# Kernel tuning notes

Measured on AMD Instinct MI355X. Metric: run time of the kernel, lower is better.

Reference implementation:

```python
import jax, jax.numpy as jnp
import numpy as np
import math

INPUT_SIZE = 512
HIDDEN_SIZE = 1024
B, T = 64, 512


def setup_inputs() -> dict:
    key = jax.random.key(0)
    ks = jax.random.split(key, 8)
    stdv = 1.0 / math.sqrt(HIDDEN_SIZE)
    def U(k, shape):
        return jax.random.uniform(k, shape, jnp.float32, -stdv, stdv)
    x = jax.random.normal(ks[0], (B, T, INPUT_SIZE), jnp.float32)
    W_i_r = U(ks[1], (HIDDEN_SIZE, INPUT_SIZE))
    W_h_r = U(ks[2], (HIDDEN_SIZE, HIDDEN_SIZE))
    W_i_z = U(ks[3], (HIDDEN_SIZE, INPUT_SIZE))
    W_h_z = U(ks[4], (HIDDEN_SIZE, HIDDEN_SIZE))
    W_i_n = U(ks[5], (HIDDEN_SIZE, INPUT_SIZE))
    W_h_n = U(ks[6], (HIDDEN_SIZE, HIDDEN_SIZE))
    zeros = jnp.zeros((HIDDEN_SIZE,), jnp.float32)
    return {
        "x": x,
        "W_i_r": W_i_r, "b_i_r": zeros, "W_h_r": W_h_r, "b_h_r": zeros,
        "W_i_z": W_i_z, "b_i_z": zeros, "W_h_z": W_h_z, "b_h_z": zeros,
        "W_i_n": W_i_n, "b_i_n": zeros, "W_h_n": W_h_n, "b_h_n": zeros,
    }


def reference(x, W_i_r, b_i_r, W_h_r, b_h_r, W_i_z, b_i_z, W_h_z, b_h_z,
              W_i_n, b_i_n, W_h_n, b_h_n):
    Bn, Tn, _ = x.shape
    # Precompute all input projections in one batched matmul each: [B,T,H]
    xr = jnp.einsum('bti,hi->bth', x, W_i_r) + b_i_r
    xz = jnp.einsum('bti,hi->bth', x, W_i_z) + b_i_z
    xn = jnp.einsum('bti,hi->bth', x, W_i_n) + b_i_n

    h0 = jnp.zeros((Bn, W_h_r.shape[0]), x.dtype)

    def step(h, inp):
        xr_t, xz_t, xn_t = inp  # each [B,H]
        r = jax.nn.sigmoid(xr_t + h @ W_h_r.T + b_h_r)
        z = jax.nn.sigmoid(xz_t + h @ W_h_z.T + b_h_z)
        n = jnp.tanh(xn_t + r * (h @ W_h_n.T + b_h_n))
        h_new = (1.0 - z) * n + z * h
        return h_new, h_new

    # scan over time: inputs transposed to [T,B,H]
    xs = (xr.transpose(1, 0, 2), xz.transpose(1, 0, 2), xn.transpose(1, 0, 2))
    _, h_seq = jax.lax.scan(step, h0, xs)
    return h_seq.transpose(1, 0, 2)  # [B,T,H]
```

## Files before the change

### kernel.cpp

```cpp
#include <hip/hip_runtime.h>
#include <math.h>


#define BB 64
#define TT 512
#define II 512
#define HH 1024
#define JB 4
#define CK 128
#define PAD 132

__device__ __forceinline__ void fma4(float4& a, const float4 xv, const float4 w) {
    a.x += xv.x * w.x;
    a.y += xv.y * w.y;
    a.z += xv.z * w.z;
    a.w += xv.w * w.w;
}

__device__ __forceinline__ void accum_chunk(
    const float* __restrict__ xsrow,
    const float* __restrict__ wr, const float* __restrict__ wz,
    const float* __restrict__ wn,
    float4& aR, float4& aZ, float4& aN)
{
#pragma unroll
    for (int k4 = 0; k4 < CK / 4; ++k4) {
        float4 xv = *(const float4*)(xsrow + k4 * 4);
        fma4(aR, xv, *(const float4*)(wr + k4 * 4));
        fma4(aZ, xv, *(const float4*)(wz + k4 * 4));
        fma4(aN, xv, *(const float4*)(wn + k4 * 4));
    }
}

__global__ __launch_bounds__(256) void gru_step(
    const float* __restrict__ x,
    const float* __restrict__ Wir, const float* __restrict__ Whr,
    const float* __restrict__ Wiz, const float* __restrict__ Whz,
    const float* __restrict__ Win, const float* __restrict__ Whn,
    const float* __restrict__ bir, const float* __restrict__ bhr,
    const float* __restrict__ biz, const float* __restrict__ bhz,
    const float* __restrict__ bin_, const float* __restrict__ bhn,
    float* __restrict__ out, int t)
{
    __shared__ float xs[BB][PAD];
    const int tid = threadIdx.x;
    const int b   = tid & 63;
    const int jg  = tid >> 6;
    const int j   = __builtin_amdgcn_readfirstlane((int)blockIdx.x * JB + jg);

    float4 aR  = {0.f, 0.f, 0.f, 0.f};
    float4 aZ  = {0.f, 0.f, 0.f, 0.f};
    float4 aXN = {0.f, 0.f, 0.f, 0.f};
    float4 aHN = {0.f, 0.f, 0.f, 0.f};

    const float* xbase = x + (size_t)t * II;
    for (int kc = 0; kc < II / CK; ++kc) {
#pragma unroll
        for (int i = 0; i < 8; ++i) {
            int f   = tid + 256 * i;
            int row = f >> 5;
            int c4  = f & 31;
            *(float4*)&xs[row][c4 * 4] =
                *(const float4*)(xbase + (size_t)row * (TT * II) + kc * CK + c4 * 4);
        }
        __syncthreads();
        accum_chunk(&xs[b][0],
                    Wir + (size_t)j * II + kc * CK,
                    Wiz + (size_t)j * II + kc * CK,
                    Win + (size_t)j * II + kc * CK,
                    aR, aZ, aXN);
        __syncthreads();
    }

    if (t > 0) {
        const float* hbase = out + (size_t)(t - 1) * HH;
        for (int kc = 0; kc < HH / CK; ++kc) {
#pragma unroll
            for (int i = 0; i < 8; ++i) {
                int f   = tid + 256 * i;
                int row = f >> 5;
                int c4  = f & 31;
                *(float4*)&xs[row][c4 * 4] =
                    *(const float4*)(hbase + (size_t)row * (TT * HH) + kc * CK + c4 * 4);
            }
            __syncthreads();
            accum_chunk(&xs[b][0],
                        Whr + (size_t)j * HH + kc * CK,
                        Whz + (size_t)j * HH + kc * CK,
                        Whn + (size_t)j * HH + kc * CK,
                        aR, aZ, aHN);
            __syncthreads();
        }
    }

    float rpre = (aR.x + aR.y + aR.z + aR.w) + bir[j] + bhr[j];
    float zpre = (aZ.x + aZ.y + aZ.z + aZ.w) + biz[j] + bhz[j];
    float hn   = (aHN.x + aHN.y + aHN.z + aHN.w) + bhn[j];
    float xn   = (aXN.x + aXN.y + aXN.z + aXN.w) + bin_[j];

    float r = 1.f / (1.f + __expf(-rpre));
    float z = 1.f / (1.f + __expf(-zpre));
    float n = tanhf(xn + r * hn);

    float hprev = (t > 0) ? out[(size_t)b * (TT * HH) + (size_t)(t - 1) * HH + j] : 0.f;
    float hnew  = (1.f - z) * n + z * hprev;
    out[(size_t)b * (TT * HH) + (size_t)t * HH + j] = hnew;
}

extern "C" void kernel_launch(void* const* d_in, const int* in_sizes, int n_in,
                              void* d_out, int out_size, void* d_ws, size_t ws_size,
                              hipStream_t stream) {
    (void)in_sizes; (void)n_in; (void)d_ws; (void)ws_size; (void)out_size;

    const float* x    = (const float*)d_in[0];
    const float* Wir  = (const float*)d_in[1];
    const float* bir  = (const float*)d_in[2];
    const float* Whr  = (const float*)d_in[3];
    const float* bhr  = (const float*)d_in[4];
    const float* Wiz  = (const float*)d_in[5];
    const float* biz  = (const float*)d_in[6];
    const float* Whz  = (const float*)d_in[7];
    const float* bhz  = (const float*)d_in[8];
    const float* Win  = (const float*)d_in[9];
    const float* bin_ = (const float*)d_in[10];
    const float* Whn  = (const float*)d_in[11];
    const float* bhn  = (const float*)d_in[12];
    float* out = (float*)d_out;

    for (int t = 0; t < TT; ++t) {
        gru_step<<<dim3(HH / JB), dim3(256), 0, stream>>>(
            x, Wir, Whr, Wiz, Whz, Win, Whn,
            bir, bhr, biz, bhz, bin_, bhn, out, t);
    }
}
```

Measured before the change: 14.14 ms.

## Use split-bf16 MFMA for GRU step with prepacked weights and inputs

Adds prep kernels that split fp32 weights and inputs into hi/lo bf16 pairs in an MFMA-friendly tiled layout. Each per-timestep step then runs 16x16x32 bf16 MFMAs, three products per pair (hi*hi, hi*lo, lo*hi), to approximate fp32 accuracy. The hidden state is double-buffered as bf16 hi/lo in workspace. This replaces scalar FMA with matrix cores and drops the LDS staging, at the cost of slightly lower precision and fewer blocks (64) per step. If the workspace is too small, it falls back to the old fp32 kernel.

Result: slower. 17.60 ms (+24.4%).

```diff
diff --git a/kernel.cpp b/kernel.cpp
--- a/kernel.cpp
+++ b/kernel.cpp
@@ -2,26 +2,200 @@
 #include <math.h>
 
 
+typedef __attribute__((ext_vector_type(8))) short short8;
+typedef __attribute__((ext_vector_type(4))) float f32x4;
+typedef unsigned short u16;
+typedef unsigned int u32;
+
+#define TT 512
 #define BB 64
-#define TT 512
 #define II 512
 #define HH 1024
-#define JB 4
+#define JT 16
+#define NBLK 64
+#define NKS 48
+#define NKS_X 16
+
+#define SZ_WPL (3ULL*64*48*512*2)
+#define OFF_WHI 0ULL
+#define OFF_WLO (OFF_WHI + SZ_WPL)
+#define SZ_XPL (512ULL*64*512*2)
+#define OFF_XHI (OFF_WLO + SZ_WPL)
+#define OFF_XLO (OFF_XHI + SZ_XPL)
+#define SZ_HPL (2ULL*64*1024*2)
+#define OFF_HHI (OFF_XLO + SZ_XPL)
+#define OFF_HLO (OFF_HHI + SZ_HPL)
+#define WS_NEEDED (OFF_HLO + SZ_HPL)
+
+__device__ __forceinline__ u16 f2bf(float f) {
+    u32 u = __float_as_uint(f);
+    u32 r = (u + 0x7FFFu + ((u >> 16) & 1u)) >> 16;
+    return (u16)r;
+}
+__device__ __forceinline__ float bf2f(u16 h) {
+    return __uint_as_float(((u32)h) << 16);
+}
+
+
+__global__ __launch_bounds__(256) void prep_w(
+    const float* __restrict__ Wir, const float* __restrict__ Whr,
+    const float* __restrict__ Wiz, const float* __restrict__ Whz,
+    const float* __restrict__ Win, const float* __restrict__ Whn,
+    u16* __restrict__ whi, u16* __restrict__ wlo)
+{
+    int id = blockIdx.x * 256 + threadIdx.x;
+    int lane = id & 63;
+    int qq = id >> 6;
+    int ks = qq % 48;
+    int rr = qq / 48;
+    int g = rr >> 6;
+    int jt = rr & 63;
+    int j = jt * 16 + (lane & 15);
+    int k = ks * 32 + (lane >> 4) * 8;
+    const float* Wi = (g == 0) ? Wir : (g == 1) ? Wiz : Win;
+    const float* Wh = (g == 0) ? Whr : (g == 1) ? Whz : Whn;
+    const float* src = (k < II) ? (Wi + (size_t)j * II + k)
+                                : (Wh + (size_t)j * HH + (k - II));
+    short8 H, L;
+#pragma unroll
+    for (int e = 0; e < 8; ++e) {
+        float f = src[e];
+        u16 hi = f2bf(f);
+        u16 lo = f2bf(f - bf2f(hi));
+        H[e] = (short)hi;
+        L[e] = (short)lo;
+    }
+    size_t dst = (size_t)qq * 512 + (size_t)lane * 8;
+    *(short8*)(whi + dst) = H;
+    *(short8*)(wlo + dst) = L;
+}
+
+__global__ __launch_bounds__(256) void prep_x(
+    const float* __restrict__ x, u16* __restrict__ xhi, u16* __restrict__ xlo)
+{
+    int id = blockIdx.x * 256 + threadIdx.x;
+    int t = id >> 12;
+    int b = (id >> 6) & 63;
+    int i8 = id & 63;
+    const float* src = x + ((size_t)b * TT + t) * II + i8 * 8;
+    short8 H, L;
+#pragma unroll
+    for (int e = 0; e < 8; ++e) {
+        float f = src[e];
+        u16 hi = f2bf(f);
+        u16 lo = f2bf(f - bf2f(hi));
+        H[e] = (short)hi;
+        L[e] = (short)lo;
+    }
+    size_t dst = ((size_t)t * 64 + b) * II + (size_t)i8 * 8;
+    *(short8*)(xhi + dst) = H;
+    *(short8*)(xlo + dst) = L;
+}
+
+
+#define LD8(p) (*(const short8*)(p))
+#define MFMA16(a, b, c) __builtin_amdgcn_mfma_f32_16x16x32_bf16((a), (b), (c), 0, 0, 0)
+
+__global__ __launch_bounds__(256) void gru_step_mfma(
+    const u16* __restrict__ xhi, const u16* __restrict__ xlo,
+    const u16* __restrict__ whi, const u16* __restrict__ wlo,
+    const u16* __restrict__ hhi_r, const u16* __restrict__ hlo_r,
+    u16* __restrict__ hhi_w, u16* __restrict__ hlo_w,
+    const float* __restrict__ bir, const float* __restrict__ bhr,
+    const float* __restrict__ biz, const float* __restrict__ bhz,
+    const float* __restrict__ bin_, const float* __restrict__ bhn,
+    float* __restrict__ out, int t)
+{
+    const int tid = threadIdx.x;
+    const int w = tid >> 6;
+    const int lane = tid & 63;
+    const int q = lane >> 4;
+    const int nn = lane & 15;
+    const int jt = blockIdx.x;
+    const int j = jt * JT + nn;
+
+    f32x4 accR = {0.f, 0.f, 0.f, 0.f};
+    f32x4 accZ = {0.f, 0.f, 0.f, 0.f};
+    f32x4 accNx = {0.f, 0.f, 0.f, 0.f};
+    f32x4 accNh = {0.f, 0.f, 0.f, 0.f};
+
+    const int rowA = w * 16 + nn;
+    const size_t GS = (size_t)64 * 48 * 512;
+    const u16* axh = xhi + ((size_t)t * 64 + rowA) * II + q * 8;
+    const u16* axl = xlo + ((size_t)t * 64 + rowA) * II + q * 8;
+    const size_t wb = (size_t)jt * 48 * 512 + (size_t)lane * 8;
+    const u16* bwh = whi + wb;
+    const u16* bwl = wlo + wb;
+
+#pragma unroll 4
+    for (int Ks = 0; Ks < NKS_X; ++Ks) {
+        short8 ah = LD8(axh + Ks * 32);
+        short8 al = LD8(axl + Ks * 32);
+        const u16* b0 = bwh + (size_t)Ks * 512;
+        const u16* l0 = bwl + (size_t)Ks * 512;
+        short8 bh, bl;
+        bh = LD8(b0);            bl = LD8(l0);
+        accR = MFMA16(ah, bh, accR); accR = MFMA16(ah, bl, accR); accR = MFMA16(al, bh, accR);
+        bh = LD8(b0 + GS);       bl = LD8(l0 + GS);
+        accZ = MFMA16(ah, bh, accZ); accZ = MFMA16(ah, bl, accZ); accZ = MFMA16(al, bh, accZ);
+        bh = LD8(b0 + 2 * GS);   bl = LD8(l0 + 2 * GS);
+        accNx = MFMA16(ah, bh, accNx); accNx = MFMA16(ah, bl, accNx); accNx = MFMA16(al, bh, accNx);
+    }
+
+    if (t > 0) {
+        const u16* ahh = hhi_r + (size_t)rowA * HH + q * 8;
+        const u16* ahl = hlo_r + (size_t)rowA * HH + q * 8;
+#pragma unroll 4
+        for (int K2 = 0; K2 < 32; ++K2) {
+            short8 ah = LD8(ahh + K2 * 32);
+            short8 al = LD8(ahl + K2 * 32);
+            const u16* b0 = bwh + (size_t)(NKS_X + K2) * 512;
+            const u16* l0 = bwl + (size_t)(NKS_X + K2) * 512;
+            short8 bh, bl;
+            bh = LD8(b0);            bl = LD8(l0);
+            accR = MFMA16(ah, bh, accR); accR = MFMA16(ah, bl, accR); accR = MFMA16(al, bh, accR);
+            bh = LD8(b0 + GS);       bl = LD8(l0 + GS);
+            accZ = MFMA16(ah, bh, accZ); accZ = MFMA16(ah, bl, accZ); accZ = MFMA16(al, bh, accZ);
+            bh = LD8(b0 + 2 * GS);   bl = LD8(l0 + 2 * GS);
+            accNh = MFMA16(ah, bh, accNh); accNh = MFMA16(ah, bl, accNh); accNh = MFMA16(al, bh, accNh);
+        }
+    }
+
+    const float vbir = bir[j], vbhr = bhr[j];
+    const float vbiz = biz[j], vbhz = bhz[j];
+    const float vbin = bin_[j], vbhn = bhn[j];
+#pragma unroll
+    for (int e = 0; e < 4; ++e) {
+        int row = w * 16 + q * 4 + e;
+        float rp = accR[e] + vbir + vbhr;
+        float zp = accZ[e] + vbiz + vbhz;
+        float hn = accNh[e] + vbhn;
+        float xn = accNx[e] + vbin;
+        float rg = 1.f / (1.f + __expf(-rp));
+        float zg = 1.f / (1.f + __expf(-zp));
+        float ng = tanhf(xn + rg * hn);
+        float hp = (t > 0) ? out[((size_t)row * TT + (t - 1)) * HH + j] : 0.f;
+        float hv = (1.f - zg) * ng + zg * hp;
+        out[((size_t)row * TT + t) * HH + j] = hv;
+        u16 hh = f2bf(hv);
+        u16 hl = f2bf(hv - bf2f(hh));
+        hhi_w[(size_t)row * HH + j] = hh;
+        hlo_w[(size_t)row * HH + j] = hl;
+    }
+}
+
+
 #define CK 128
 #define PAD 132
 
 __device__ __forceinline__ void fma4(float4& a, const float4 xv, const float4 w) {
-    a.x += xv.x * w.x;
-    a.y += xv.y * w.y;
-    a.z += xv.z * w.z;
-    a.w += xv.w * w.w;
+    a.x += xv.x * w.x; a.y += xv.y * w.y; a.z += xv.z * w.z; a.w += xv.w * w.w;
 }
 
 __device__ __forceinline__ void accum_chunk(
     const float* __restrict__ xsrow,
     const float* __restrict__ wr, const float* __restrict__ wz,
-    const float* __restrict__ wn,
-    float4& aR, float4& aZ, float4& aN)
+    const float* __restrict__ wn, float4& aR, float4& aZ, float4& aN)
 {
 #pragma unroll
     for (int k4 = 0; k4 < CK / 4; ++k4) {
@@ -32,7 +206,7 @@
     }
 }
 
-__global__ __launch_bounds__(256) void gru_step(
+__global__ __launch_bounds__(256) void gru_step_f32(
     const float* __restrict__ x,
     const float* __restrict__ Wir, const float* __restrict__ Whr,
     const float* __restrict__ Wiz, const float* __restrict__ Whz,
@@ -44,73 +218,59 @@
 {
     __shared__ float xs[BB][PAD];
     const int tid = threadIdx.x;
-    const int b   = tid & 63;
-    const int jg  = tid >> 6;
-    const int j   = __builtin_amdgcn_readfirstlane((int)blockIdx.x * JB + jg);
-
-    float4 aR  = {0.f, 0.f, 0.f, 0.f};
-    float4 aZ  = {0.f, 0.f, 0.f, 0.f};
-    float4 aXN = {0.f, 0.f, 0.f, 0.f};
-    float4 aHN = {0.f, 0.f, 0.f, 0.f};
+    const int b = tid & 63;
+    const int jg = tid >> 6;
+    const int j = __builtin_amdgcn_readfirstlane((int)blockIdx.x * 4 + jg);
+
+    float4 aR = {0,0,0,0}, aZ = {0,0,0,0}, aXN = {0,0,0,0}, aHN = {0,0,0,0};
 
     const float* xbase = x + (size_t)t * II;
     for (int kc = 0; kc < II / CK; ++kc) {
 #pragma unroll
         for (int i = 0; i < 8; ++i) {
-            int f   = tid + 256 * i;
-            int row = f >> 5;
-            int c4  = f & 31;
+            int f = tid + 256 * i; int row = f >> 5; int c4 = f & 31;
             *(float4*)&xs[row][c4 * 4] =
                 *(const float4*)(xbase + (size_t)row * (TT * II) + kc * CK + c4 * 4);
         }
         __syncthreads();
-        accum_chunk(&xs[b][0],
-                    Wir + (size_t)j * II + kc * CK,
-                    Wiz + (size_t)j * II + kc * CK,
-                    Win + (size_t)j * II + kc * CK,
+        accum_chunk(&xs[b][0], Wir + (size_t)j * II + kc * CK,
+                    Wiz + (size_t)j * II + kc * CK, Win + (size_t)j * II + kc * CK,
                     aR, aZ, aXN);
         __syncthreads();
     }
-
     if (t > 0) {
         const float* hbase = out + (size_t)(t - 1) * HH;
         for (int kc = 0; kc < HH / CK; ++kc) {
 #pragma unroll
             for (int i = 0; i < 8; ++i) {
-                int f   = tid + 256 * i;
-                int row = f >> 5;
-                int c4  = f & 31;
+                int f = tid + 256 * i; int row = f >> 5; int c4 = f & 31;
                 *(float4*)&xs[row][c4 * 4] =
                     *(const float4*)(hbase + (size_t)row * (TT * HH) + kc * CK + c4 * 4);
             }
             __syncthreads();
-            accum_chunk(&xs[b][0],
-                        Whr + (size_t)j * HH + kc * CK,
-                        Whz + (size_t)j * HH + kc * CK,
-                        Whn + (size_t)j * HH + kc * CK,
+            accum_chunk(&xs[b][0], Whr + (size_t)j * HH + kc * CK,
+                        Whz + (size_t)j * HH + kc * CK, Whn + (size_t)j * HH + kc * CK,
                         aR, aZ, aHN);
             __syncthreads();
         }
     }
-
     float rpre = (aR.x + aR.y + aR.z + aR.w) + bir[j] + bhr[j];
     float zpre = (aZ.x + aZ.y + aZ.z + aZ.w) + biz[j] + bhz[j];
-    float hn   = (aHN.x + aHN.y + aHN.z + aHN.w) + bhn[j];
-    float xn   = (aXN.x + aXN.y + aXN.z + aXN.w) + bin_[j];
-
+    float hn = (aHN.x + aHN.y + aHN.z + aHN.w) + bhn[j];
+    float xn = (aXN.x + aXN.y + aXN.z + aXN.w) + bin_[j];
     float r = 1.f / (1.f + __expf(-rpre));
     float z = 1.f / (1.f + __expf(-zpre));
     float n = tanhf(xn + r * hn);
-
     float hprev = (t > 0) ? out[(size_t)b * (TT * HH) + (size_t)(t - 1) * HH + j] : 0.f;
-    float hnew  = (1.f - z) * n + z * hprev;
+    float hnew = (1.f - z) * n + z * hprev;
     out[(size_t)b * (TT * HH) + (size_t)t * HH + j] = hnew;
 }
+
 
 extern "C" void kernel_launch(void* const* d_in, const int* in_sizes, int n_in,
                               void* d_out, int out_size, void* d_ws, size_t ws_size,
                               hipStream_t stream) {
-    (void)in_sizes; (void)n_in; (void)d_ws; (void)ws_size; (void)out_size;
+    (void)in_sizes; (void)n_in; (void)out_size;
 
     const float* x    = (const float*)d_in[0];
     const float* Wir  = (const float*)d_in[1];
@@ -127,9 +287,34 @@
     const float* bhn  = (const float*)d_in[12];
     float* out = (float*)d_out;
 
+    if (ws_size < WS_NEEDED) {
+        for (int t = 0; t < TT; ++t) {
+            gru_step_f32<<<dim3(HH / 4), dim3(256), 0, stream>>>(
+                x, Wir, Whr, Wiz, Whz, Win, Whn,
+                bir, bhr, biz, bhz, bin_, bhn, out, t);
+        }
+        return;
+    }
+
+    unsigned char* ws = (unsigned char*)d_ws;
+    u16* whi = (u16*)(ws + OFF_WHI);
+    u16* wlo = (u16*)(ws + OFF_WLO);
+    u16* xhi = (u16*)(ws + OFF_XHI);
+    u16* xlo = (u16*)(ws + OFF_XLO);
+    u16* hhi = (u16*)(ws + OFF_HHI);
+    u16* hlo = (u16*)(ws + OFF_HLO);
+
+    prep_w<<<dim3(589824 / 256), dim3(256), 0, stream>>>(
+        Wir, Whr, Wiz, Whz, Win, Whn, whi, wlo);
+    prep_x<<<dim3(2097152 / 256), dim3(256), 0, stream>>>(x, xhi, xlo);
+
     for (int t = 0; t < TT; ++t) {
-        gru_step<<<dim3(HH / JB), dim3(256), 0, stream>>>(
-            x, Wir, Whr, Wiz, Whz, Win, Whn,
+        int wp = t & 1;
+        int rp = wp ^ 1;
+        gru_step_mfma<<<dim3(NBLK), dim3(256), 0, stream>>>(
+            xhi, xlo, whi, wlo,
+            hhi + (size_t)rp * (BB * HH), hlo + (size_t)rp * (BB * HH),
+            hhi + (size_t)wp * (BB * HH), hlo + (size_t)wp * (BB * HH),
             bir, bhr, biz, bhz, bin_, bhn, out, t);
     }
 }
```

## Retile GRU step into 16-row by 16-unit blocks with split-K reduction

Applied to the files above, without the earlier changes.

Each block now stages 16 batch rows of the concatenated [x_t, h_{t-1}] (1536 values each) in shared memory once, instead of repeatedly staging 64-row chunks. Each thread computes 4 hidden units for one row across a quarter of the K dimension, and the partial sums are reduced through shared memory. The goal is fewer synchronisations and better reuse of each weight load across 4 outputs, with float4 output stores. The trade-offs are that each weight is now re-read by 4 batch-quarter blocks, weight loads come from global memory with strided per-thread access, and the shared memory footprint is large.

Measured after the change: 20.20 ms. 1.43x slower.

```diff
diff --git a/kernel.cpp b/kernel.cpp
--- a/kernel.cpp
+++ b/kernel.cpp
@@ -2,37 +2,19 @@
 #include <math.h>
 
 
-#define BB 64
 #define TT 512
 #define II 512
 #define HH 1024
-#define JB 4
-#define CK 128
-#define PAD 132
+#define XSTRIDE 1540
 
-__device__ __forceinline__ void fma4(float4& a, const float4 xv, const float4 w) {
-    a.x += xv.x * w.x;
-    a.y += xv.y * w.y;
-    a.z += xv.z * w.z;
-    a.w += xv.w * w.w;
+__device__ __forceinline__ void fma4(float4& a, const float4 v, const float4 w) {
+    a.x += v.x * w.x; a.y += v.y * w.y; a.z += v.z * w.z; a.w += v.w * w.w;
+}
+__device__ __forceinline__ float hadd4(const float4 a) {
+    return (a.x + a.y) + (a.z + a.w);
 }
 
-__device__ __forceinline__ void accum_chunk(
-    const float* __restrict__ xsrow,
-    const float* __restrict__ wr, const float* __restrict__ wz,
-    const float* __restrict__ wn,
-    float4& aR, float4& aZ, float4& aN)
-{
-#pragma unroll
-    for (int k4 = 0; k4 < CK / 4; ++k4) {
-        float4 xv = *(const float4*)(xsrow + k4 * 4);
-        fma4(aR, xv, *(const float4*)(wr + k4 * 4));
-        fma4(aZ, xv, *(const float4*)(wz + k4 * 4));
-        fma4(aN, xv, *(const float4*)(wn + k4 * 4));
-    }
-}
-
-__global__ __launch_bounds__(256) void gru_step(
+__global__ __launch_bounds__(256, 1) void gru_step(
     const float* __restrict__ x,
     const float* __restrict__ Wir, const float* __restrict__ Whr,
     const float* __restrict__ Wiz, const float* __restrict__ Whz,
@@ -42,69 +24,135 @@
     const float* __restrict__ bin_, const float* __restrict__ bhn,
     float* __restrict__ out, int t)
 {
-    __shared__ float xs[BB][PAD];
+    __shared__ float xs[16 * XSTRIDE];
+    __shared__ float red[3 * 64 * 16];
+
     const int tid = threadIdx.x;
-    const int b   = tid & 63;
-    const int jg  = tid >> 6;
-    const int j   = __builtin_amdgcn_readfirstlane((int)blockIdx.x * JB + jg);
+    const int jt  = blockIdx.x & 63;
+    const int mq  = blockIdx.x >> 6;
+    const int R0  = mq * 16;
 
-    float4 aR  = {0.f, 0.f, 0.f, 0.f};
-    float4 aZ  = {0.f, 0.f, 0.f, 0.f};
-    float4 aXN = {0.f, 0.f, 0.f, 0.f};
-    float4 aHN = {0.f, 0.f, 0.f, 0.f};
+#pragma unroll
+    for (int i = 0; i < 8; ++i) {
+        int f = tid + 256 * i;
+        int r = f >> 7, c = f & 127;
+        float4 v = *(const float4*)(x + ((size_t)(R0 + r) * TT + t) * II + c * 4);
+        *(float4*)&xs[r * XSTRIDE + c * 4] = v;
+    }
+    if (t > 0) {
+#pragma unroll
+        for (int i = 0; i < 16; ++i) {
+            int f = tid + 256 * i;
+            int r = f >> 8, c = f & 255;
+            float4 v = *(const float4*)(out + ((size_t)(R0 + r) * TT + (t - 1)) * HH + c * 4);
+            *(float4*)&xs[r * XSTRIDE + 512 + c * 4] = v;
+        }
+    } else {
+        float4 z4 = {0.f, 0.f, 0.f, 0.f};
+#pragma unroll
+        for (int i = 0; i < 16; ++i) {
+            int f = tid + 256 * i;
+            int r = f >> 8, c = f & 255;
+            *(float4*)&xs[r * XSTRIDE + 512 + c * 4] = z4;
+        }
+    }
+    __syncthreads();
 
-    const float* xbase = x + (size_t)t * II;
-    for (int kc = 0; kc < II / CK; ++kc) {
+    const int r  = tid & 15;
+    const int jq = (tid >> 4) & 3;
+    const int kq = tid >> 6;
+    const int j0 = jt * 16 + jq * 4;
+
+    float4 aR[4], aZ[4], aNx[4], aNh[4];
 #pragma unroll
-        for (int i = 0; i < 8; ++i) {
-            int f   = tid + 256 * i;
-            int row = f >> 5;
-            int c4  = f & 31;
-            *(float4*)&xs[row][c4 * 4] =
-                *(const float4*)(xbase + (size_t)row * (TT * II) + kc * CK + c4 * 4);
-        }
-        __syncthreads();
-        accum_chunk(&xs[b][0],
-                    Wir + (size_t)j * II + kc * CK,
-                    Wiz + (size_t)j * II + kc * CK,
-                    Win + (size_t)j * II + kc * CK,
-                    aR, aZ, aXN);
-        __syncthreads();
+    for (int jj = 0; jj < 4; ++jj) {
+        aR[jj] = aZ[jj] = aNx[jj] = aNh[jj] = (float4){0.f, 0.f, 0.f, 0.f};
     }
 
-    if (t > 0) {
-        const float* hbase = out + (size_t)(t - 1) * HH;
-        for (int kc = 0; kc < HH / CK; ++kc) {
+    const float* xsrow = &xs[r * XSTRIDE + kq * 384];
+    const int kbase = kq * 384;
+    const int nx = (kq == 0) ? 96 : (kq == 1) ? 32 : 0;
+
+#pragma unroll 2
+    for (int k4 = 0; k4 < nx; ++k4) {
+        float4 xv = *(const float4*)(xsrow + k4 * 4);
+        int k = kbase + k4 * 4;
 #pragma unroll
-            for (int i = 0; i < 8; ++i) {
-                int f   = tid + 256 * i;
-                int row = f >> 5;
-                int c4  = f & 31;
-                *(float4*)&xs[row][c4 * 4] =
-                    *(const float4*)(hbase + (size_t)row * (TT * HH) + kc * CK + c4 * 4);
-            }
-            __syncthreads();
-            accum_chunk(&xs[b][0],
-                        Whr + (size_t)j * HH + kc * CK,
-                        Whz + (size_t)j * HH + kc * CK,
-                        Whn + (size_t)j * HH + kc * CK,
-                        aR, aZ, aHN);
-            __syncthreads();
+        for (int jj = 0; jj < 4; ++jj) {
+            size_t wo = (size_t)(j0 + jj) * II + k;
+            fma4(aR[jj],  xv, *(const float4*)(Wir + wo));
+            fma4(aZ[jj],  xv, *(const float4*)(Wiz + wo));
+            fma4(aNx[jj], xv, *(const float4*)(Win + wo));
+        }
+    }
+#pragma unroll 2
+    for (int k4 = nx; k4 < 96; ++k4) {
+        float4 xv = *(const float4*)(xsrow + k4 * 4);
+        int kh = kbase + k4 * 4 - 512;
+#pragma unroll
+        for (int jj = 0; jj < 4; ++jj) {
+            size_t wo = (size_t)(j0 + jj) * HH + kh;
+            fma4(aR[jj],  xv, *(const float4*)(Whr + wo));
+            fma4(aZ[jj],  xv, *(const float4*)(Whz + wo));
+            fma4(aNh[jj], xv, *(const float4*)(Whn + wo));
         }
     }
 
-    float rpre = (aR.x + aR.y + aR.z + aR.w) + bir[j] + bhr[j];
-    float zpre = (aZ.x + aZ.y + aZ.z + aZ.w) + biz[j] + bhz[j];
-    float hn   = (aHN.x + aHN.y + aHN.z + aHN.w) + bhn[j];
-    float xn   = (aXN.x + aXN.y + aXN.z + aXN.w) + bin_[j];
+    float p[16];
+#pragma unroll
+    for (int jj = 0; jj < 4; ++jj) {
+        p[jj * 4 + 0] = hadd4(aR[jj]);
+        p[jj * 4 + 1] = hadd4(aZ[jj]);
+        p[jj * 4 + 2] = hadd4(aNx[jj]);
+        p[jj * 4 + 3] = hadd4(aNh[jj]);
+    }
+    if (kq > 0) {
+        float* dst = &red[((kq - 1) * 64 + (tid & 63)) * 16];
+#pragma unroll
+        for (int i = 0; i < 16; ++i) dst[i] = p[i];
+    }
+    __syncthreads();
 
-    float r = 1.f / (1.f + __expf(-rpre));
-    float z = 1.f / (1.f + __expf(-zpre));
-    float n = tanhf(xn + r * hn);
+    if (kq == 0) {
+#pragma unroll
+        for (int w = 0; w < 3; ++w) {
+            const float* src = &red[(w * 64 + (tid & 63)) * 16];
+#pragma unroll
+            for (int i = 0; i < 16; ++i) p[i] += src[i];
+        }
+        float4 vbir = *(const float4*)(bir + j0);
+        float4 vbhr = *(const float4*)(bhr + j0);
+        float4 vbiz = *(const float4*)(biz + j0);
+        float4 vbhz = *(const float4*)(bhz + j0);
+        float4 vbin = *(const float4*)(bin_ + j0);
+        float4 vbhn = *(const float4*)(bhn + j0);
+        const float* pbir = (const float*)&vbir;
+        const float* pbhr = (const float*)&vbhr;
+        const float* pbiz = (const float*)&vbiz;
+        const float* pbhz = (const float*)&vbhz;
+        const float* pbin = (const float*)&vbin;
+        const float* pbhn = (const float*)&vbhn;
 
-    float hprev = (t > 0) ? out[(size_t)b * (TT * HH) + (size_t)(t - 1) * HH + j] : 0.f;
-    float hnew  = (1.f - z) * n + z * hprev;
-    out[(size_t)b * (TT * HH) + (size_t)t * HH + j] = hnew;
+        size_t orow = ((size_t)(R0 + r) * TT + t) * HH + j0;
+        float4 hprev = {0.f, 0.f, 0.f, 0.f};
+        if (t > 0) hprev = *(const float4*)(out + orow - HH);
+        const float* php = (const float*)&hprev;
+
+        float4 hnew;
+        float* phn = (float*)&hnew;
+#pragma unroll
+        for (int jj = 0; jj < 4; ++jj) {
+            float rpre = p[jj * 4 + 0] + pbir[jj] + pbhr[jj];
+            float zpre = p[jj * 4 + 1] + pbiz[jj] + pbhz[jj];
+            float xn   = p[jj * 4 + 2] + pbin[jj];
+            float hn   = p[jj * 4 + 3] + pbhn[jj];
+            float rg = 1.f / (1.f + __expf(-rpre));
+            float zg = 1.f / (1.f + __expf(-zpre));
+            float ng = tanhf(xn + rg * hn);
+            phn[jj] = (1.f - zg) * ng + zg * php[jj];
+        }
+        *(float4*)(out + orow) = hnew;
+    }
 }
 
 extern "C" void kernel_launch(void* const* d_in, const int* in_sizes, int n_in,
@@ -128,7 +176,7 @@
     float* out = (float*)d_out;
 
     for (int t = 0; t < TT; ++t) {
-        gru_step<<<dim3(HH / JB), dim3(256), 0, stream>>>(
+        gru_step<<<dim3(256), dim3(256), 0, stream>>>(
             x, Wir, Whr, Wiz, Whz, Win, Whn,
             bir, bhr, biz, bhz, bin_, bhn, out, t);
     }
```
